# Kernel tuning notes

Measured on AMD Instinct MI355X. Metric: run time of the kernel, lower is better.

The kernel has to match this reference:

```python
import jax, jax.numpy as jnp
import numpy as np

N_SYM = 128
BATCH = 131072
LEVERAGE = 30.0


def setup_inputs() -> dict:
    key = jax.random.key(0)
    ks = jax.random.split(key, 8)
    fractions = jax.random.normal(ks[0], (N_SYM, BATCH), dtype=jnp.float32)
    # exec_samples are Bernoulli(0/1) execution indicators, kept as float
    exec_samples = jnp.round(jax.random.uniform(ks[1], (N_SYM, BATCH), dtype=jnp.float32))
    pos_sizes = jax.random.normal(ks[2], (N_SYM, BATCH), dtype=jnp.float32)
    # margin rates strictly positive
    margin_rates = jax.random.uniform(ks[3], (N_SYM, BATCH), dtype=jnp.float32) * 0.9 + 0.1
    unused_margin = jax.random.uniform(ks[4], (BATCH,), dtype=jnp.float32) * 1000.0
    # per-symbol volume constraints: min == step (typical broker config), max >> min
    msm_step = jax.random.uniform(ks[5], (N_SYM,), dtype=jnp.float32) * 0.01 + 0.01
    msm_min = msm_step
    msm_max = msm_step * 1000.0
    return {
        "fractions": fractions,
        "exec_samples": exec_samples,
        "pos_sizes": pos_sizes,
        "margin_rates": margin_rates,
        "unused_margin": unused_margin,
        "msm_min": msm_min,
        "msm_step": msm_step,
        "msm_max": msm_max,
    }


def reference(fractions, exec_samples, pos_sizes, margin_rates, unused_margin,
              msm_min, msm_step, msm_max):
    """JAX port of LowLevelInferenceEngine._compute_new_pos_sizes.

    Sequential recurrence over traded symbols (axis 0), carrying
    unused_margin [BATCH]. Returns (new_pos_sizes [N_SYM, BATCH],
    final unused_margin [BATCH]).
    """

    def step_fn(um, xs):
        frac, ex, pos, mr, mn, st, mx = xs
        unused_size = um * mr * LEVERAGE
        max_pos_size = jnp.abs(pos) + unused_size
        # torch.where(pos*frac > 0, unused_size, max_pos_size).minimum(0)
        adj = jnp.minimum(jnp.where(pos * frac > 0, unused_size, max_pos_size), 0.0)
        new_pos_size = frac * (max_pos_size - adj)
        abs_nps = jnp.abs(new_pos_size)
        sgn = jnp.sign(new_pos_size)
        abs_nps = jnp.floor(abs_nps / st) * st
        abs_nps = jnp.where(abs_nps < mn, 0.0, abs_nps)
        abs_nps = jnp.minimum(abs_nps, mx)
        out = ex * (sgn * abs_nps) + (1.0 - ex) * pos
        um_new = (max_pos_size - abs_nps) / (mr * LEVERAGE)
        return um_new, out

    um_final, new_pos_sizes = jax.lax.scan(
        step_fn,
        unused_margin,
        (fractions, exec_samples, pos_sizes, margin_rates, msm_min, msm_step, msm_max),
    )
    return new_pos_sizes, um_final
```

## Files before the change

### kernel.cpp

```cpp
#include <hip/hip_runtime.h>
#include <math.h>

#define N_SYM 128
#define BATCH 131072
#define B4    (BATCH / 4)
#define LEV   30.0f
#define D     8

typedef float v4 __attribute__((ext_vector_type(4)));

__device__ __forceinline__ float step1(float f, float e, float p, float m,
                                       float st, float mn, float mx,
                                       float* um)
{
    const float mrl = m * LEV;
    const float us  = *um * mrl;
    const float mps = fabsf(p) + us;
    const float adj = fminf((p * f > 0.0f) ? us : mps, 0.0f);
    const float nps = f * (mps - adj);

    float       a  = fabsf(nps);
    const float sg = copysignf(1.0f, nps);
    a = floorf(a / st) * st;
    a = (a < mn) ? 0.0f : a;
    a = fminf(a, mx);

    *um = (mps - a) / mrl;
    return e * (sg * a) + (1.0f - e) * p;
}

__global__ __launch_bounds__(64) void lle_scan_kernel(
    const float* __restrict__ frac,
    const float* __restrict__ exs,
    const float* __restrict__ pos,
    const float* __restrict__ mrate,
    const float* __restrict__ um0,
    const float* __restrict__ msm_min,
    const float* __restrict__ msm_step,
    const float* __restrict__ msm_max,
    float* __restrict__ out)
{
    const size_t c4 = (size_t)(blockIdx.x * 64 + threadIdx.x);

    const v4* F = (const v4*)frac;
    const v4* E = (const v4*)exs;
    const v4* P = (const v4*)pos;
    const v4* M = (const v4*)mrate;
    v4*       O = (v4*)out;

    const v4 umv = __builtin_nontemporal_load((const v4*)um0 + c4);
    float um[4] = {umv.x, umv.y, umv.z, umv.w};

    v4 fb[D], eb[D], pb[D], mb[D];

#pragma unroll
    for (int j = 0; j < D; ++j) {
        const size_t o = (size_t)j * B4 + c4;
        fb[j] = __builtin_nontemporal_load(F + o);
        eb[j] = __builtin_nontemporal_load(E + o);
        pb[j] = __builtin_nontemporal_load(P + o);
        mb[j] = __builtin_nontemporal_load(M + o);
    }

    for (int s0 = 0; s0 < N_SYM - D; s0 += D) {
#pragma unroll
        for (int j = 0; j < D; ++j) {
            const int s = s0 + j;
            const v4 f = fb[j];
            const v4 e = eb[j];
            const v4 p = pb[j];
            const v4 m = mb[j];

            {
                const size_t o = (size_t)(s + D) * B4 + c4;
                fb[j] = __builtin_nontemporal_load(F + o);
                eb[j] = __builtin_nontemporal_load(E + o);
                pb[j] = __builtin_nontemporal_load(P + o);
                mb[j] = __builtin_nontemporal_load(M + o);
            }

            const float st = msm_step[s];
            const float mn = msm_min[s];
            const float mx = msm_max[s];

            v4 r;
            r.x = step1(f.x, e.x, p.x, m.x, st, mn, mx, &um[0]);
            r.y = step1(f.y, e.y, p.y, m.y, st, mn, mx, &um[1]);
            r.z = step1(f.z, e.z, p.z, m.z, st, mn, mx, &um[2]);
            r.w = step1(f.w, e.w, p.w, m.w, st, mn, mx, &um[3]);

            __builtin_nontemporal_store(r, O + (size_t)s * B4 + c4);
        }
    }

#pragma unroll
    for (int j = 0; j < D; ++j) {
        const int s = N_SYM - D + j;
        const v4 f = fb[j];
        const v4 e = eb[j];
        const v4 p = pb[j];
        const v4 m = mb[j];

        const float st = msm_step[s];
        const float mn = msm_min[s];
        const float mx = msm_max[s];

        v4 r;
        r.x = step1(f.x, e.x, p.x, m.x, st, mn, mx, &um[0]);
        r.y = step1(f.y, e.y, p.y, m.y, st, mn, mx, &um[1]);
        r.z = step1(f.z, e.z, p.z, m.z, st, mn, mx, &um[2]);
        r.w = step1(f.w, e.w, p.w, m.w, st, mn, mx, &um[3]);

        __builtin_nontemporal_store(r, O + (size_t)s * B4 + c4);
    }

    v4 umo;
    umo.x = um[0]; umo.y = um[1]; umo.z = um[2]; umo.w = um[3];
    __builtin_nontemporal_store(umo, O + (size_t)N_SYM * B4 + c4);
}

extern "C" void kernel_launch(void* const* d_in, const int* in_sizes, int n_in,
                              void* d_out, int out_size, void* d_ws, size_t ws_size,
                              hipStream_t stream) {
    const float* frac     = (const float*)d_in[0];
    const float* exs      = (const float*)d_in[1];
    const float* pos      = (const float*)d_in[2];
    const float* mrate    = (const float*)d_in[3];
    const float* um0      = (const float*)d_in[4];
    const float* msm_min  = (const float*)d_in[5];
    const float* msm_step = (const float*)d_in[6];
    const float* msm_max  = (const float*)d_in[7];
    float* out = (float*)d_out;

    const int block = 64;
    const int grid  = (BATCH / 4) / block;

    hipLaunchKernelGGL(lle_scan_kernel, dim3(grid), dim3(block), 0, stream,
                       frac, exs, pos, mrate, um0, msm_min, msm_step, msm_max,
                       out);
}
```

Baseline: 259.1 us.

## Split into producer wave streaming via global_load_lds and consumer compute wave

Replaces the per-thread register prefetch ring with a warp-specialized design. One wave issues direct global-to-LDS loads into a 4-slot ring buffer, and a second wave reads the data from LDS, runs the sequential scan and stores the results. The two waves synchronize with s_barrier and hand-tuned vmcnt waits. The aim is to keep more loads in flight without spending consumer registers. In exchange it adds a barrier per phase and LDS traffic, and the waitcnt counts must match the issued load count exactly or the consumer reads stale data.

```diff
diff --git a/kernel.cpp b/kernel.cpp
--- a/kernel.cpp
+++ b/kernel.cpp
@@ -1,13 +1,23 @@
 #include <hip/hip_runtime.h>
 #include <math.h>
 
-#define N_SYM 128
-#define BATCH 131072
-#define B4    (BATCH / 4)
-#define LEV   30.0f
-#define D     8
+#define N_SYM  128
+#define BATCH  131072
+#define B4     (BATCH / 4)
+#define LEV    30.0f
+#define SLOT   4
+#define NSLOT  4
+#define PHASES (N_SYM / SLOT)
 
 typedef float v4 __attribute__((ext_vector_type(4)));
+
+__device__ __forceinline__ void gload16(const void* g, void* l)
+{
+    __builtin_amdgcn_global_load_lds(
+        (const __attribute__((address_space(1))) void*)g,
+        (__attribute__((address_space(3))) void*)l,
+        16, 0, 0);
+}
 
 __device__ __forceinline__ float step1(float f, float e, float p, float m,
                                        float st, float mn, float mx,
@@ -29,7 +39,7 @@
     return e * (sg * a) + (1.0f - e) * p;
 }
 
-__global__ __launch_bounds__(64) void lle_scan_kernel(
+__global__ __launch_bounds__(128) void lle_pc_kernel(
     const float* __restrict__ frac,
     const float* __restrict__ exs,
     const float* __restrict__ pos,
@@ -40,7 +50,11 @@
     const float* __restrict__ msm_max,
     float* __restrict__ out)
 {
-    const size_t c4 = (size_t)(blockIdx.x * 64 + threadIdx.x);
+    __shared__ v4 lds_buf[NSLOT][SLOT][4][64];
+
+    const int    wave = threadIdx.x >> 6;
+    const int    lane = threadIdx.x & 63;
+    const size_t c4   = (size_t)blockIdx.x * 64 + lane;
 
     const v4* F = (const v4*)frac;
     const v4* E = (const v4*)exs;
@@ -48,75 +62,76 @@
     const v4* M = (const v4*)mrate;
     v4*       O = (v4*)out;
 
-    const v4 umv = __builtin_nontemporal_load((const v4*)um0 + c4);
-    float um[4] = {umv.x, umv.y, umv.z, umv.w};
+    if (wave == 1) {
+#define ISSUE_SLOT(SL)                                                    \
+        {                                                                 \
+            const int _ring = (SL) & (NSLOT - 1);                         \
+            _Pragma("unroll")                                             \
+            for (int _j = 0; _j < SLOT; ++_j) {                           \
+                const size_t _ro = (size_t)((SL) * SLOT + _j) * B4 + c4;  \
+                gload16(F + _ro, &lds_buf[_ring][_j][0][0]);              \
+                gload16(E + _ro, &lds_buf[_ring][_j][1][0]);              \
+                gload16(P + _ro, &lds_buf[_ring][_j][2][0]);              \
+                gload16(M + _ro, &lds_buf[_ring][_j][3][0]);              \
+            }                                                             \
+        }
 
-    v4 fb[D], eb[D], pb[D], mb[D];
+        ISSUE_SLOT(0);
+        ISSUE_SLOT(1);
+        ISSUE_SLOT(2);
+        asm volatile("s_waitcnt vmcnt(32)" ::: "memory");
+        __builtin_amdgcn_s_barrier();
 
+        for (int p = 0; p < PHASES - 3; ++p) {
+            ISSUE_SLOT(p + 3);
+            asm volatile("s_waitcnt vmcnt(32)" ::: "memory");
+            __builtin_amdgcn_s_barrier();
+        }
+        asm volatile("s_waitcnt vmcnt(16)" ::: "memory");
+        __builtin_amdgcn_s_barrier();
+        asm volatile("s_waitcnt vmcnt(0)" ::: "memory");
+        __builtin_amdgcn_s_barrier();
+#undef ISSUE_SLOT
+    } else {
+        const v4 umv = *((const v4*)um0 + c4);
+        float um[4] = {umv.x, umv.y, umv.z, umv.w};
+
+        __builtin_amdgcn_s_barrier();
+        asm volatile("" ::: "memory");
+
+        for (int p = 0; p < PHASES; ++p) {
+            const int ring = p & (NSLOT - 1);
 #pragma unroll
-    for (int j = 0; j < D; ++j) {
-        const size_t o = (size_t)j * B4 + c4;
-        fb[j] = __builtin_nontemporal_load(F + o);
-        eb[j] = __builtin_nontemporal_load(E + o);
-        pb[j] = __builtin_nontemporal_load(P + o);
-        mb[j] = __builtin_nontemporal_load(M + o);
+            for (int j = 0; j < SLOT; ++j) {
+                const int s = p * SLOT + j;
+                const v4 f  = lds_buf[ring][j][0][lane];
+                const v4 e  = lds_buf[ring][j][1][lane];
+                const v4 pv = lds_buf[ring][j][2][lane];
+                const v4 m  = lds_buf[ring][j][3][lane];
+
+                const float st = msm_step[s];
+                const float mn = msm_min[s];
+                const float mx = msm_max[s];
+
+                v4 r;
+                r.x = step1(f.x, e.x, pv.x, m.x, st, mn, mx, &um[0]);
+                r.y = step1(f.y, e.y, pv.y, m.y, st, mn, mx, &um[1]);
+                r.z = step1(f.z, e.z, pv.z, m.z, st, mn, mx, &um[2]);
+                r.w = step1(f.w, e.w, pv.w, m.w, st, mn, mx, &um[3]);
+
+                __builtin_nontemporal_store(r, O + (size_t)s * B4 + c4);
+            }
+            if (p < PHASES - 1) {
+                asm volatile("s_waitcnt lgkmcnt(0)" ::: "memory");
+                __builtin_amdgcn_s_barrier();
+                asm volatile("" ::: "memory");
+            }
+        }
+
+        v4 umo;
+        umo.x = um[0]; umo.y = um[1]; umo.z = um[2]; umo.w = um[3];
+        __builtin_nontemporal_store(umo, O + (size_t)N_SYM * B4 + c4);
     }
-
-    for (int s0 = 0; s0 < N_SYM - D; s0 += D) {
-#pragma unroll
-        for (int j = 0; j < D; ++j) {
-            const int s = s0 + j;
-            const v4 f = fb[j];
-            const v4 e = eb[j];
-            const v4 p = pb[j];
-            const v4 m = mb[j];
-
-            {
-                const size_t o = (size_t)(s + D) * B4 + c4;
-                fb[j] = __builtin_nontemporal_load(F + o);
-                eb[j] = __builtin_nontemporal_load(E + o);
-                pb[j] = __builtin_nontemporal_load(P + o);
-                mb[j] = __builtin_nontemporal_load(M + o);
-            }
-
-            const float st = msm_step[s];
-            const float mn = msm_min[s];
-            const float mx = msm_max[s];
-
-            v4 r;
-            r.x = step1(f.x, e.x, p.x, m.x, st, mn, mx, &um[0]);
-            r.y = step1(f.y, e.y, p.y, m.y, st, mn, mx, &um[1]);
-            r.z = step1(f.z, e.z, p.z, m.z, st, mn, mx, &um[2]);
-            r.w = step1(f.w, e.w, p.w, m.w, st, mn, mx, &um[3]);
-
-            __builtin_nontemporal_store(r, O + (size_t)s * B4 + c4);
-        }
-    }
-
-#pragma unroll
-    for (int j = 0; j < D; ++j) {
-        const int s = N_SYM - D + j;
-        const v4 f = fb[j];
-        const v4 e = eb[j];
-        const v4 p = pb[j];
-        const v4 m = mb[j];
-
-        const float st = msm_step[s];
-        const float mn = msm_min[s];
-        const float mx = msm_max[s];
-
-        v4 r;
-        r.x = step1(f.x, e.x, p.x, m.x, st, mn, mx, &um[0]);
-        r.y = step1(f.y, e.y, p.y, m.y, st, mn, mx, &um[1]);
-        r.z = step1(f.z, e.z, p.z, m.z, st, mn, mx, &um[2]);
-        r.w = step1(f.w, e.w, p.w, m.w, st, mn, mx, &um[3]);
-
-        __builtin_nontemporal_store(r, O + (size_t)s * B4 + c4);
-    }
-
-    v4 umo;
-    umo.x = um[0]; umo.y = um[1]; umo.z = um[2]; umo.w = um[3];
-    __builtin_nontemporal_store(umo, O + (size_t)N_SYM * B4 + c4);
 }
 
 extern "C" void kernel_launch(void* const* d_in, const int* in_sizes, int n_in,
@@ -132,10 +147,10 @@
     const float* msm_max  = (const float*)d_in[7];
     float* out = (float*)d_out;
 
-    const int block = 64;
-    const int grid  = (BATCH / 4) / block;
+    const int block = 128;
+    const int grid  = (BATCH / 4) / 64;
 
-    hipLaunchKernelGGL(lle_scan_kernel, dim3(grid), dim3(block), 0, stream,
+    hipLaunchKernelGGL(lle_pc_kernel, dim3(grid), dim3(block), 0, stream,
                        frac, exs, pos, mrate, um0, msm_min, msm_step, msm_max,
                        out);
 }
```

After: 272.9 us. 5.3% more time.

## Stage inputs through LDS with async global_load_lds ring buffer in 512-thread blocks

Applied to the files above, without the earlier changes.

Replaces per-thread register prefetching of 4-wide vectors with cooperative 512-thread blocks where each wave-pair loads one input array directly into an LDS ring buffer via global_load_lds. Each thread then processes one column, reading from LDS behind vmcnt waits and barriers, with two phases of four symbols prefetched ahead. The aim is deeper, register-free memory pipelining to raise achieved bandwidth. In exchange it adds block-wide barriers per phase and relies on hand-counted vmcnt values.

```diff
diff --git a/kernel.cpp b/kernel.cpp
--- a/kernel.cpp
+++ b/kernel.cpp
@@ -3,11 +3,18 @@
 
 #define N_SYM 128
 #define BATCH 131072
-#define B4    (BATCH / 4)
 #define LEV   30.0f
-#define D     8
+#define CPB   512
+#define SPP   4
+#define NPH   (N_SYM / SPP)
 
-typedef float v4 __attribute__((ext_vector_type(4)));
+__device__ __forceinline__ void gload16(const float* g, float* l)
+{
+    __builtin_amdgcn_global_load_lds(
+        (const __attribute__((address_space(1))) void*)g,
+        (__attribute__((address_space(3))) void*)l,
+        16, 0, 0);
+}
 
 __device__ __forceinline__ float step1(float f, float e, float p, float m,
                                        float st, float mn, float mx,
@@ -29,7 +36,11 @@
     return e * (sg * a) + (1.0f - e) * p;
 }
 
-__global__ __launch_bounds__(64) void lle_scan_kernel(
+#define VMWAIT(N) asm volatile("s_waitcnt vmcnt(" #N ")" ::: "memory")
+#define BARRIER() do { __builtin_amdgcn_s_barrier(); \
+                       asm volatile("" ::: "memory"); } while (0)
+
+__global__ __launch_bounds__(512) void lle_coop_kernel(
     const float* __restrict__ frac,
     const float* __restrict__ exs,
     const float* __restrict__ pos,
@@ -40,83 +51,63 @@
     const float* __restrict__ msm_max,
     float* __restrict__ out)
 {
-    const size_t c4 = (size_t)(blockIdx.x * 64 + threadIdx.x);
+    __shared__ float lds[4 * SPP * 4 * CPB];
 
-    const v4* F = (const v4*)frac;
-    const v4* E = (const v4*)exs;
-    const v4* P = (const v4*)pos;
-    const v4* M = (const v4*)mrate;
-    v4*       O = (v4*)out;
+    const int t     = threadIdx.x;
+    const int wave  = t >> 6;
+    const int lane  = t & 63;
+    const int gcol0 = blockIdx.x * CPB;
 
-    const v4 umv = __builtin_nontemporal_load((const v4*)um0 + c4);
-    float um[4] = {umv.x, umv.y, umv.z, umv.w};
+    const int aidx = wave >> 1;
+    const float* src = (aidx == 0) ? frac : (aidx == 1) ? exs
+                     : (aidx == 2) ? pos  : mrate;
+    const size_t scol = (size_t)gcol0 + (size_t)((wave & 1) * 256 + lane * 4);
+    const int    wlds = aidx * 512 + (wave & 1) * 256;
 
-    v4 fb[D], eb[D], pb[D], mb[D];
+    auto issue = [&](int slot) {
+        const int rb = (slot & 3) * 8192 + wlds;
+#pragma unroll
+        for (int j = 0; j < SPP; ++j)
+            gload16(src + (size_t)(slot * SPP + j) * BATCH + scol,
+                    &lds[rb + j * 2048]);
+    };
 
+    float um = um0[gcol0 + t];
+
+    auto compute = [&](int k) {
+        const int rb = (k & 3) * 8192;
 #pragma unroll
-    for (int j = 0; j < D; ++j) {
-        const size_t o = (size_t)j * B4 + c4;
-        fb[j] = __builtin_nontemporal_load(F + o);
-        eb[j] = __builtin_nontemporal_load(E + o);
-        pb[j] = __builtin_nontemporal_load(P + o);
-        mb[j] = __builtin_nontemporal_load(M + o);
-    }
-
-    for (int s0 = 0; s0 < N_SYM - D; s0 += D) {
-#pragma unroll
-        for (int j = 0; j < D; ++j) {
-            const int s = s0 + j;
-            const v4 f = fb[j];
-            const v4 e = eb[j];
-            const v4 p = pb[j];
-            const v4 m = mb[j];
-
-            {
-                const size_t o = (size_t)(s + D) * B4 + c4;
-                fb[j] = __builtin_nontemporal_load(F + o);
-                eb[j] = __builtin_nontemporal_load(E + o);
-                pb[j] = __builtin_nontemporal_load(P + o);
-                mb[j] = __builtin_nontemporal_load(M + o);
-            }
-
+        for (int j = 0; j < SPP; ++j) {
+            const int   s  = k * SPP + j;
             const float st = msm_step[s];
             const float mn = msm_min[s];
             const float mx = msm_max[s];
+            const float f  = lds[rb + j * 2048 +        t];
+            const float e  = lds[rb + j * 2048 +  512 + t];
+            const float pv = lds[rb + j * 2048 + 1024 + t];
+            const float m  = lds[rb + j * 2048 + 1536 + t];
+            const float r  = step1(f, e, pv, m, st, mn, mx, &um);
+            __builtin_nontemporal_store(r, &out[(size_t)s * BATCH + gcol0 + t]);
+        }
+    };
 
-            v4 r;
-            r.x = step1(f.x, e.x, p.x, m.x, st, mn, mx, &um[0]);
-            r.y = step1(f.y, e.y, p.y, m.y, st, mn, mx, &um[1]);
-            r.z = step1(f.z, e.z, p.z, m.z, st, mn, mx, &um[2]);
-            r.w = step1(f.w, e.w, p.w, m.w, st, mn, mx, &um[3]);
+    issue(0);
+    issue(1);
 
-            __builtin_nontemporal_store(r, O + (size_t)s * B4 + c4);
-        }
+    issue(2);  VMWAIT(8);  BARRIER();  compute(0);
+    issue(3);  VMWAIT(12); BARRIER();  compute(1);
+
+    for (int k = 2; k <= NPH - 3; ++k) {
+        issue(k + 2);
+        VMWAIT(16);
+        BARRIER();
+        compute(k);
     }
 
-#pragma unroll
-    for (int j = 0; j < D; ++j) {
-        const int s = N_SYM - D + j;
-        const v4 f = fb[j];
-        const v4 e = eb[j];
-        const v4 p = pb[j];
-        const v4 m = mb[j];
+    VMWAIT(12); BARRIER(); compute(30);
+    VMWAIT(8);  BARRIER(); compute(31);
 
-        const float st = msm_step[s];
-        const float mn = msm_min[s];
-        const float mx = msm_max[s];
-
-        v4 r;
-        r.x = step1(f.x, e.x, p.x, m.x, st, mn, mx, &um[0]);
-        r.y = step1(f.y, e.y, p.y, m.y, st, mn, mx, &um[1]);
-        r.z = step1(f.z, e.z, p.z, m.z, st, mn, mx, &um[2]);
-        r.w = step1(f.w, e.w, p.w, m.w, st, mn, mx, &um[3]);
-
-        __builtin_nontemporal_store(r, O + (size_t)s * B4 + c4);
-    }
-
-    v4 umo;
-    umo.x = um[0]; umo.y = um[1]; umo.z = um[2]; umo.w = um[3];
-    __builtin_nontemporal_store(umo, O + (size_t)N_SYM * B4 + c4);
+    __builtin_nontemporal_store(um, &out[(size_t)N_SYM * BATCH + gcol0 + t]);
 }
 
 extern "C" void kernel_launch(void* const* d_in, const int* in_sizes, int n_in,
@@ -132,10 +123,10 @@
     const float* msm_max  = (const float*)d_in[7];
     float* out = (float*)d_out;
 
-    const int block = 64;
-    const int grid  = (BATCH / 4) / block;
+    const int block = 512;
+    const int grid  = BATCH / CPB;
 
-    hipLaunchKernelGGL(lle_scan_kernel, dim3(grid), dim3(block), 0, stream,
+    hipLaunchKernelGGL(lle_coop_kernel, dim3(grid), dim3(block), 0, stream,
                        frac, exs, pos, mrate, um0, msm_min, msm_step, msm_max,
                        out);
 }
```

Result: slower. 269.0 us (+3.8%).
